# Kernel optimization log

Hardware: AMD Instinct MI355X
Metric: run time of the kernel (lower is better)

The kernel has to match this reference:

```python
import jax, jax.numpy as jnp
import numpy as np

EPS = 1e-12  # F.normalize eps
WIN_SIZE = 200
WIN_STEP = 30  # eval mode (training uses 10)
N_WIN = 30     # 31 windows from length-1100 axis, last one dropped


def setup_inputs() -> dict:
    key = jax.random.key(0)
    ks = jax.random.split(key, 6)
    dim, K, out_dim = 128, 64, 256
    N, H, W = 8, 16, 900
    s = 1.0 / np.sqrt(dim)
    return {
        "x": jax.random.normal(ks[0], (N, dim, H, W), dtype=jnp.float32),
        "cluster_centers": jax.random.uniform(ks[1], (K, dim), dtype=jnp.float32),
        "conv_w": jax.random.normal(ks[2], (K, dim), dtype=jnp.float32) * s,
        "conv_b": jax.random.normal(ks[3], (K,), dtype=jnp.float32) * s,
        "mlp_w": jax.random.normal(ks[4], (out_dim, K * dim), dtype=jnp.float32) * s,
        "mlp_b": jax.random.normal(ks[5], (out_dim,), dtype=jnp.float32) * s,
    }


def _l2norm(v, axis):
    return v / jnp.clip(jnp.linalg.norm(v, axis=axis, keepdims=True), EPS)


def reference(x, cluster_centers, conv_w, conv_b, mlp_w, mlp_b):
    N, C, H, W = x.shape
    K = conv_w.shape[0]
    # 1x1 conv -> soft assignment, softmax over clusters (dim=1 after view(N,K,HW))
    logits = jnp.einsum('nchw,kc->nkhw', x, conv_w) + conv_b[None, :, None, None]
    a = jax.nn.softmax(logits, axis=1)  # (N,K,H,W)
    # Fused weighted residual sum over H (torch sums dim=-2 of (N,K,C,H,W)):
    # vlad_pre[n,k,c,w] = sum_h a[n,k,h,w]*x[n,c,h,w] - centers[k,c]*sum_h a[n,k,h,w]
    wx = jnp.einsum('nkhw,nchw->nkcw', a, x)               # (N,K,C,W)
    asum = a.sum(axis=2)                                    # (N,K,W)
    res = wx - cluster_centers[None, :, :, None] * asum[:, :, None, :]
    # circular pad along yaw: [800:] ++ all ++ [:100] -> length 1100
    res = jnp.concatenate([res[..., 800:], res, res[..., :100]], axis=-1)
    # sliding-window sum, size 200 step 30, drop last window -> 30 windows
    cs = jnp.cumsum(res, axis=-1)
    cs = jnp.concatenate([jnp.zeros(res.shape[:-1] + (1,), res.dtype), cs], axis=-1)
    starts = jnp.arange(N_WIN) * WIN_STEP
    win = cs[..., starts + WIN_SIZE] - cs[..., starts]      # (N,K,C,30)
    vlad = jnp.transpose(win, (0, 3, 1, 2)).reshape(N * N_WIN, K, C)
    vlad = _l2norm(vlad, axis=2)                            # intra-norm per cluster
    vlad = _l2norm(vlad.reshape(N * N_WIN, K * C), axis=1)  # global norm
    out = vlad @ mlp_w.T + mlp_b
    out = _l2norm(out, axis=1)
    return out.reshape(N, N_WIN, -1)
```

## Files before the change

kernel.cpp:

```cpp
#include <hip/hip_runtime.h>
#include <cstddef>

#define EPSF 1e-12f
#define NCB 90
#define NT 30
#define ODIM 256
#define DDIM 8192

typedef unsigned short u16;
typedef __attribute__((ext_vector_type(8))) short short8;
typedef __attribute__((ext_vector_type(4))) float float4v;

__device__ inline u16 f2bf(float f) {
  union { float f; unsigned u; } v; v.f = f;
  unsigned r = v.u + 0x7FFFu + ((v.u >> 16) & 1u);
  return (u16)(r >> 16);
}
__device__ inline float bf2f(u16 h) {
  union { unsigned u; float f; } v; v.u = ((unsigned)h) << 16;
  return v.f;
}

__global__ __launch_bounds__(256, 3) void k1_assign(
    const float* __restrict__ x,
    const float* __restrict__ conv_w,
    const float* __restrict__ conv_b,
    float* __restrict__ P,
    float* __restrict__ PA)
{
  __shared__ u16 xtf[4160];
  __shared__ u16 xf[5120];
  __shared__ float As[64 * 33];
  __shared__ u16 afr[2048];
  __shared__ float invs[32];
  __shared__ float pasum[256];

  const int bx0 = blockIdx.x;
  const int id = (bx0 & 7) * 90 + (bx0 >> 3);
  const int n = id / NCB, cb = id - n * NCB;
  const int t = threadIdx.x;
  const int lane = t & 63;
  const int w = t >> 6;

  const float* xn = x + (size_t)n * 1843200 + cb * 10;

  const int colt = w & 1;
  const int kt0 = w >> 1;
  const float bk0 = conv_b[kt0 * 16 + (lane & 15)];
  const float bk1 = conv_b[(kt0 + 2) * 16 + (lane & 15)];

  short8 w0h[4], w0l[4], w1h[4], w1l[4];
  {
    int kr0 = kt0 * 16 + (lane & 15);
    int kr1 = kr0 + 32;
    int cbase = (lane >> 4) << 3;
#pragma unroll
    for (int cb32 = 0; cb32 < 4; ++cb32) {
      const float* wp0 = conv_w + (size_t)kr0 * 128 + cb32 * 32 + cbase;
      const float* wp1 = conv_w + (size_t)kr1 * 128 + cb32 * 32 + cbase;
      union { u16 u[8]; short8 v; } hh, ll;
#pragma unroll
      for (int j = 0; j < 8; ++j) {
        float fv = wp0[j];
        u16 h = f2bf(fv);
        hh.u[j] = h;
        ll.u[j] = f2bf(fv - bf2f(h));
      }
      w0h[cb32] = hh.v; w0l[cb32] = ll.v;
#pragma unroll
      for (int j = 0; j < 8; ++j) {
        float fv = wp1[j];
        u16 h = f2bf(fv);
        hh.u[j] = h;
        ll.u[j] = f2bf(fv - bf2f(h));
      }
      w1h[cb32] = hh.v; w1l[cb32] = ll.v;
    }
  }

  float4v pacc[8];
#pragma unroll
  for (int i = 0; i < 8; ++i) pacc[i] = (float4v){0.f, 0.f, 0.f, 0.f};
  float pak = 0.f;

  float2 xr[8];
#pragma unroll
  for (int s = 0; s < 8; ++s) {
    int e2 = t + 256 * s;
    int c = e2 >> 4, p = e2 & 15;
    int cl = 2 * p;
    int h = cl / 10, wi = cl - 10 * h;
    xr[s] = *(const float2*)(xn + (size_t)c * 14400 + h * 900 + wi);
  }

  for (int cc = 0; cc < 5; ++cc) {
    __syncthreads();
#pragma unroll
    for (int s = 0; s < 8; ++s) {
      int e2 = t + 256 * s;
      int c = e2 >> 4, p = e2 & 15;
      int cl = 2 * p;
      u16 h0 = f2bf(xr[s].x), h1 = f2bf(xr[s].y);
      int ip = (c >> 4) * 640 + (p >> 2) * 160 + (c & 15) * 8 + (cl & 7);
      ushort2 pr; pr.x = h0; pr.y = h1;
      *(ushort2*)&xf[ip] = pr;
      int F = (p >> 3) * 4 + (c >> 5);
      int L = (((c >> 3) & 3) << 4) + (cl & 15);
      int i0 = F * 520 + L * 8 + (c & 7);
      xtf[i0] = h0;
      xtf[i0 + 8] = h1;
    }
    if (cc < 4) {
#pragma unroll
      for (int s = 0; s < 8; ++s) {
        int e2 = t + 256 * s;
        int c = e2 >> 4, p = e2 & 15;
        int g = (cc + 1) * 32 + 2 * p;
        int h = g / 10, wi = g - 10 * h;
        xr[s] = *(const float2*)(xn + (size_t)c * 14400 + h * 900 + wi);
      }
    }
    __syncthreads();

    {
      float4v d0 = (float4v){0.f, 0.f, 0.f, 0.f};
      float4v d1 = (float4v){0.f, 0.f, 0.f, 0.f};
#pragma unroll
      for (int cb32 = 0; cb32 < 4; ++cb32) {
        short8 xa = *(short8*)&xtf[(colt * 4 + cb32) * 520 + lane * 8];
        d0 = __builtin_amdgcn_mfma_f32_16x16x32_bf16(xa, w0h[cb32], d0, 0, 0, 0);
        d0 = __builtin_amdgcn_mfma_f32_16x16x32_bf16(xa, w0l[cb32], d0, 0, 0, 0);
        d1 = __builtin_amdgcn_mfma_f32_16x16x32_bf16(xa, w1h[cb32], d1, 0, 0, 0);
        d1 = __builtin_amdgcn_mfma_f32_16x16x32_bf16(xa, w1l[cb32], d1, 0, 0, 0);
      }
      int colb = colt * 16 + ((lane >> 4) << 2);
      int kr0 = kt0 * 16 + (lane & 15);
      int kr1 = kr0 + 32;
#pragma unroll
      for (int r = 0; r < 4; ++r) {
        As[kr0 * 33 + colb + r] = d0[r] + bk0;
        As[kr1 * 33 + colb + r] = d1[r] + bk1;
      }
    }
    __syncthreads();

    {
      const int col8 = lane & 7;
      const int kq = lane >> 3;
      const int colg = w * 8 + col8;
      float m = -3.4e38f;
#pragma unroll
      for (int i = 0; i < 8; ++i) m = fmaxf(m, As[(kq * 8 + i) * 33 + colg]);
      m = fmaxf(m, __shfl_xor(m, 8));
      m = fmaxf(m, __shfl_xor(m, 16));
      m = fmaxf(m, __shfl_xor(m, 32));
      float s = 0.f;
#pragma unroll
      for (int i = 0; i < 8; ++i) {
        int a = (kq * 8 + i) * 33 + colg;
        float e = __expf(As[a] - m);
        As[a] = e;
        s += e;
      }
      s += __shfl_xor(s, 8);
      s += __shfl_xor(s, 16);
      s += __shfl_xor(s, 32);
      if (kq == 0) invs[w * 8 + col8] = 1.f / s;
    }
    {
      union { u16 u[8]; short8 v; } cvt;
      float paks = 0.f;
#pragma unroll
      for (int j = 0; j < 8; ++j) {
        float a = As[lane * 33 + w * 8 + j] * invs[w * 8 + j];
        paks += a;
        cvt.u[j] = f2bf(a);
      }
      pak += paks;
      int dst = ((lane >> 4) * 64 + (w << 4) + (lane & 15)) * 8;
      *(short8*)&afr[dst] = cvt.v;
    }
    __syncthreads();

    {
      short8 aa = *(short8*)&afr[(w * 64 + lane) * 8];
#pragma unroll
      for (int ct = 0; ct < 8; ++ct) {
        short8 xb = *(short8*)&xf[ct * 640 + (lane >> 4) * 160 + (lane & 15) * 8];
        pacc[ct] = __builtin_amdgcn_mfma_f32_16x16x32_bf16(aa, xb, pacc[ct], 0, 0, 0);
      }
    }
  }

  float* Pp = P + (size_t)(n * NCB + cb) * DDIM;
  {
    int krow = w * 16 + ((lane >> 4) << 2);
    int c0 = lane & 15;
#pragma unroll
    for (int ct = 0; ct < 8; ++ct)
#pragma unroll
      for (int r = 0; r < 4; ++r)
        Pp[(krow + r) * 128 + ct * 16 + c0] = pacc[ct][r];
  }
  pasum[t] = pak;
  __syncthreads();
  if (t < 64)
    PA[(size_t)(n * NCB + cb) * 64 + t] =
        pasum[t] + pasum[64 + t] + pasum[128 + t] + pasum[192 + t];
}

__global__ __launch_bounds__(256) void k2_vlad(
    const float* __restrict__ P, const float* __restrict__ PA,
    const float* __restrict__ centers, u16* __restrict__ vlad16,
    float* __restrict__ gss)
{
  __shared__ float Ak[8];
  __shared__ float red[4];
  const int bx0 = blockIdx.x;
  const int id = (bx0 & 7) * 240 + (bx0 >> 3);
  const int n = id / 240;
  const int rem = id - n * 240;
  const int wt = rem >> 3, eb = rem & 7;
  const int win = n * NT + wt;
  const int t = threadIdx.x;

  if (t < 32) {
    int kk = t >> 2, ii = t & 3;
    float s = 0.f;
#pragma unroll
    for (int ss = 0; ss < 5; ++ss) {
      int i = ii + 4 * ss;
      int cb = (3 * wt + 80 + i) % 90;
      s += PA[((size_t)n * NCB + cb) * 64 + eb * 8 + kk];
    }
    s += __shfl_xor(s, 1);
    s += __shfl_xor(s, 2);
    if (ii == 0) Ak[kk] = s;
  }
  __syncthreads();

  const int e0 = eb * 1024 + t * 4;
  const float* base = P + (size_t)n * NCB * DDIM + e0;
  float v[4];
#pragma unroll
  for (int j = 0; j < 4; ++j) v[j] = 0.f;
#pragma unroll 5
  for (int i = 0; i < 20; ++i) {
    int cb = (3 * wt + 80 + i) % 90;
    float4 u0 = *(const float4*)(base + (size_t)cb * DDIM);
    v[0] += u0.x; v[1] += u0.y; v[2] += u0.z; v[3] += u0.w;
  }

  const float A = Ak[t >> 5];
  const float* ce = centers + e0;
  float ss8 = 0.f;
#pragma unroll
  for (int j = 0; j < 4; ++j) {
    float val = v[j] - ce[j] * A;
    v[j] = val;
    ss8 += val * val;
  }
  float ssg = ss8;
  ssg += __shfl_xor(ssg, 1);
  ssg += __shfl_xor(ssg, 2);
  ssg += __shfl_xor(ssg, 4);
  ssg += __shfl_xor(ssg, 8);
  ssg += __shfl_xor(ssg, 16);
  float rn = 1.f / fmaxf(sqrtf(ssg), EPSF);
  float ts = ss8 * rn * rn;
  ts += __shfl_xor(ts, 1);
  ts += __shfl_xor(ts, 2);
  ts += __shfl_xor(ts, 4);
  ts += __shfl_xor(ts, 8);
  ts += __shfl_xor(ts, 16);
  ts += __shfl_xor(ts, 32);
  if ((t & 63) == 0) red[t >> 6] = ts;
  __syncthreads();
  if (t == 0) gss[(size_t)win * 8 + eb] = red[0] + red[1] + red[2] + red[3];

  union { u16 u[4]; ushort4 v4; } o;
#pragma unroll
  for (int j = 0; j < 4; ++j) o.u[j] = f2bf(v[j] * rn);
  *(ushort4*)(vlad16 + (size_t)win * DDIM + e0) = o.v4;
}

__global__ __launch_bounds__(256) void k3_gemm(
    const u16* __restrict__ vlad16, const float* __restrict__ gss,
    const float* __restrict__ mlp_w, float* __restrict__ part)
{
  __shared__ float ga[48];
  const int bx = blockIdx.x;
  const int xcd = bx & 7;
  const int q = bx >> 3;
  const int rtg = q % 5;
  const int h = (q / 5) * 8 + xcd;
  const int ot = h & 1;
  const int ks = h >> 1;
  const int t = threadIdx.x;
  const int lane = t & 63;
  const int w = t >> 6;

  if (t < 48) {
    int r = rtg * 48 + t;
    float s = 0.f;
#pragma unroll
    for (int j = 0; j < 8; ++j) s += gss[(size_t)r * 8 + j];
    ga[t] = 1.f / fmaxf(sqrtf(s), EPSF);
  }
  __syncthreads();

  const int m = lane & 15;
  const int kg = lane >> 4;
  const int d0 = ks * 256 + kg * 8;
  const u16* a0 = vlad16 + (size_t)(rtg * 48 + m) * DDIM + d0;

  float4v acc[3][2];
#pragma unroll
  for (int mi = 0; mi < 3; ++mi)
#pragma unroll
    for (int i = 0; i < 2; ++i) acc[mi][i] = (float4v){0.f, 0.f, 0.f, 0.f};

#pragma unroll
  for (int ko = 0; ko < 8; ++ko) {
    short8 a[3];
#pragma unroll
    for (int mi = 0; mi < 3; ++mi)
      a[mi] = *(const short8*)(a0 + (size_t)(mi * 16) * DDIM + ko * 32);
#pragma unroll
    for (int nt = 0; nt < 2; ++nt) {
      int o = ot * 128 + w * 32 + nt * 16 + m;
      const float* wrow = mlp_w + (size_t)o * DDIM + d0 + ko * 32;
      float4 u0 = *(const float4*)wrow;
      float4 u1 = *(const float4*)(wrow + 4);
      union { u16 u[8]; short8 v; } bb;
      bb.u[0] = f2bf(u0.x); bb.u[1] = f2bf(u0.y); bb.u[2] = f2bf(u0.z); bb.u[3] = f2bf(u0.w);
      bb.u[4] = f2bf(u1.x); bb.u[5] = f2bf(u1.y); bb.u[6] = f2bf(u1.z); bb.u[7] = f2bf(u1.w);
#pragma unroll
      for (int mi = 0; mi < 3; ++mi)
        acc[mi][nt] = __builtin_amdgcn_mfma_f32_16x16x32_bf16(a[mi], bb.v, acc[mi][nt], 0, 0, 0);
    }
  }

  float* pp = part + ((size_t)ks * 240 + rtg * 48) * ODIM;
#pragma unroll
  for (int mi = 0; mi < 3; ++mi)
#pragma unroll
    for (int nt = 0; nt < 2; ++nt) {
      int o = ot * 128 + w * 32 + nt * 16 + m;
#pragma unroll
      for (int r = 0; r < 4; ++r) {
        int rl = mi * 16 + kg * 4 + r;
        pp[rl * ODIM + o] = acc[mi][nt][r] * ga[rl];
      }
    }
}

__global__ __launch_bounds__(1024) void k4_out(
    const float* __restrict__ part, const float* __restrict__ bias,
    float* __restrict__ out)
{
  __shared__ float acc[4][256];
  __shared__ float red[4];
  const int r = blockIdx.x;
  const int t = threadIdx.x;
  const int o = t & 255, sq = t >> 8;

  float v = 0.f;
#pragma unroll
  for (int s = 0; s < 8; ++s)
    v += part[((size_t)(sq * 8 + s) * 240 + r) * ODIM + o];
  acc[sq][o] = v;
  __syncthreads();

  float ss = 0.f;
  if (t < 256) {
    v = acc[0][o] + acc[1][o] + acc[2][o] + acc[3][o] + bias[o];
    ss = v * v;
    ss += __shfl_xor(ss, 32);
    ss += __shfl_xor(ss, 16);
    ss += __shfl_xor(ss, 8);
    ss += __shfl_xor(ss, 4);
    ss += __shfl_xor(ss, 2);
    ss += __shfl_xor(ss, 1);
    if ((t & 63) == 0) red[t >> 6] = ss;
  }
  __syncthreads();
  if (t < 256) {
    float total = red[0] + red[1] + red[2] + red[3];
    out[(size_t)r * ODIM + o] = v / fmaxf(sqrtf(total), EPSF);
  }
}

extern "C" void kernel_launch(void* const* d_in, const int* in_sizes, int n_in,
                              void* d_out, int out_size, void* d_ws, size_t ws_size,
                              hipStream_t stream) {
  const float* x       = (const float*)d_in[0];
  const float* centers = (const float*)d_in[1];
  const float* conv_w  = (const float*)d_in[2];
  const float* conv_b  = (const float*)d_in[3];
  const float* mlp_w   = (const float*)d_in[4];
  const float* mlp_b   = (const float*)d_in[5];
  float* out = (float*)d_out;

  float* ws     = (float*)d_ws;
  float* P      = ws;
  float* PA     = ws + 5898240;
  u16*   vlad16 = (u16*)(ws + 5944320);
  float* gss    = (float*)(ws + 6927360);
  float* part   = ws;

  k1_assign<<<dim3(8 * NCB),    dim3(256),  0, stream>>>(x, conv_w, conv_b, P, PA);
  k2_vlad  <<<dim3(8 * NT * 8), dim3(256),  0, stream>>>(P, PA, centers, vlad16, gss);
  k3_gemm  <<<dim3(320),        dim3(256),  0, stream>>>(vlad16, gss, mlp_w, part);
  k4_out   <<<dim3(240),        dim3(1024), 0, stream>>>(part, mlp_b, out);
}
```

Measured before the change: 172.2 us.

## Split k1_assign work across 8 waves with 512-thread blocks

Doubles k1_assign's block size from 256 to 512 threads and splits per-wave work in half. Each wave now computes one 16-cluster tile of logits, handles 4 columns in the softmax, and runs 4 of the 8 channel tiles in the weighted-sum MFMA. Weight loading uses float4 vector loads, and the block-index mapping to (n, cb) is simplified. The aim is more waves per block to hide latency and lighter register pressure per thread, at the cost of larger blocks, possibly fewer resident blocks per CU, and an extra shuffle stage in the softmax.

```diff
diff --git a/kernel.cpp b/kernel.cpp
--- a/kernel.cpp
+++ b/kernel.cpp
@@ -21,7 +21,7 @@
   return v.f;
 }
 
-__global__ __launch_bounds__(256, 3) void k1_assign(
+__global__ __launch_bounds__(512, 2) void k1_assign(
     const float* __restrict__ x,
     const float* __restrict__ conv_w,
     const float* __restrict__ conv_b,
@@ -33,60 +33,51 @@
   __shared__ float As[64 * 33];
   __shared__ u16 afr[2048];
   __shared__ float invs[32];
-  __shared__ float pasum[256];
+  __shared__ float pasum[512];
 
   const int bx0 = blockIdx.x;
-  const int id = (bx0 & 7) * 90 + (bx0 >> 3);
-  const int n = id / NCB, cb = id - n * NCB;
+  const int n = bx0 & 7;
+  const int cb = bx0 >> 3;
   const int t = threadIdx.x;
   const int lane = t & 63;
-  const int w = t >> 6;
+  const int w8 = t >> 6;
 
   const float* xn = x + (size_t)n * 1843200 + cb * 10;
 
-  const int colt = w & 1;
-  const int kt0 = w >> 1;
-  const float bk0 = conv_b[kt0 * 16 + (lane & 15)];
-  const float bk1 = conv_b[(kt0 + 2) * 16 + (lane & 15)];
-
-  short8 w0h[4], w0l[4], w1h[4], w1l[4];
+  const int colt = w8 & 1;
+  const int kt = w8 >> 1;
+  const int kr = kt * 16 + (lane & 15);
+  const float bk = conv_b[kr];
+
+  short8 wh[4], wl[4];
   {
-    int kr0 = kt0 * 16 + (lane & 15);
-    int kr1 = kr0 + 32;
-    int cbase = (lane >> 4) << 3;
+    const int cbase = (lane >> 4) << 3;
 #pragma unroll
     for (int cb32 = 0; cb32 < 4; ++cb32) {
-      const float* wp0 = conv_w + (size_t)kr0 * 128 + cb32 * 32 + cbase;
-      const float* wp1 = conv_w + (size_t)kr1 * 128 + cb32 * 32 + cbase;
+      const float* wp = conv_w + (size_t)kr * 128 + cb32 * 32 + cbase;
+      float4 u0 = *(const float4*)wp;
+      float4 u1 = *(const float4*)(wp + 4);
+      float fv[8] = {u0.x, u0.y, u0.z, u0.w, u1.x, u1.y, u1.z, u1.w};
       union { u16 u[8]; short8 v; } hh, ll;
 #pragma unroll
       for (int j = 0; j < 8; ++j) {
-        float fv = wp0[j];
-        u16 h = f2bf(fv);
+        u16 h = f2bf(fv[j]);
         hh.u[j] = h;
-        ll.u[j] = f2bf(fv - bf2f(h));
-      }
-      w0h[cb32] = hh.v; w0l[cb32] = ll.v;
-#pragma unroll
-      for (int j = 0; j < 8; ++j) {
-        float fv = wp1[j];
-        u16 h = f2bf(fv);
-        hh.u[j] = h;
-        ll.u[j] = f2bf(fv - bf2f(h));
-      }
-      w1h[cb32] = hh.v; w1l[cb32] = ll.v;
-    }
-  }
-
-  float4v pacc[8];
-#pragma unroll
-  for (int i = 0; i < 8; ++i) pacc[i] = (float4v){0.f, 0.f, 0.f, 0.f};
+        ll.u[j] = f2bf(fv[j] - bf2f(h));
+      }
+      wh[cb32] = hh.v; wl[cb32] = ll.v;
+    }
+  }
+
+  float4v pacc[4];
+#pragma unroll
+  for (int i = 0; i < 4; ++i) pacc[i] = (float4v){0.f, 0.f, 0.f, 0.f};
   float pak = 0.f;
 
-  float2 xr[8];
-#pragma unroll
-  for (int s = 0; s < 8; ++s) {
-    int e2 = t + 256 * s;
+  float2 xr[4];
+#pragma unroll
+  for (int s = 0; s < 4; ++s) {
+    int e2 = t + 512 * s;
     int c = e2 >> 4, p = e2 & 15;
     int cl = 2 * p;
     int h = cl / 10, wi = cl - 10 * h;
@@ -96,8 +87,8 @@
   for (int cc = 0; cc < 5; ++cc) {
     __syncthreads();
 #pragma unroll
-    for (int s = 0; s < 8; ++s) {
-      int e2 = t + 256 * s;
+    for (int s = 0; s < 4; ++s) {
+      int e2 = t + 512 * s;
       int c = e2 >> 4, p = e2 & 15;
       int cl = 2 * p;
       u16 h0 = f2bf(xr[s].x), h1 = f2bf(xr[s].y);
@@ -112,8 +103,8 @@
     }
     if (cc < 4) {
 #pragma unroll
-      for (int s = 0; s < 8; ++s) {
-        int e2 = t + 256 * s;
+      for (int s = 0; s < 4; ++s) {
+        int e2 = t + 512 * s;
         int c = e2 >> 4, p = e2 & 15;
         int g = (cc + 1) * 32 + 2 * p;
         int h = g / 10, wi = g - 10 * h;
@@ -124,89 +115,88 @@
 
     {
       float4v d0 = (float4v){0.f, 0.f, 0.f, 0.f};
-      float4v d1 = (float4v){0.f, 0.f, 0.f, 0.f};
 #pragma unroll
       for (int cb32 = 0; cb32 < 4; ++cb32) {
         short8 xa = *(short8*)&xtf[(colt * 4 + cb32) * 520 + lane * 8];
-        d0 = __builtin_amdgcn_mfma_f32_16x16x32_bf16(xa, w0h[cb32], d0, 0, 0, 0);
-        d0 = __builtin_amdgcn_mfma_f32_16x16x32_bf16(xa, w0l[cb32], d0, 0, 0, 0);
-        d1 = __builtin_amdgcn_mfma_f32_16x16x32_bf16(xa, w1h[cb32], d1, 0, 0, 0);
-        d1 = __builtin_amdgcn_mfma_f32_16x16x32_bf16(xa, w1l[cb32], d1, 0, 0, 0);
+        d0 = __builtin_amdgcn_mfma_f32_16x16x32_bf16(xa, wh[cb32], d0, 0, 0, 0);
+        d0 = __builtin_amdgcn_mfma_f32_16x16x32_bf16(xa, wl[cb32], d0, 0, 0, 0);
       }
       int colb = colt * 16 + ((lane >> 4) << 2);
-      int kr0 = kt0 * 16 + (lane & 15);
-      int kr1 = kr0 + 32;
-#pragma unroll
-      for (int r = 0; r < 4; ++r) {
-        As[kr0 * 33 + colb + r] = d0[r] + bk0;
-        As[kr1 * 33 + colb + r] = d1[r] + bk1;
-      }
+#pragma unroll
+      for (int r = 0; r < 4; ++r)
+        As[kr * 33 + colb + r] = d0[r] + bk;
     }
     __syncthreads();
 
     {
-      const int col8 = lane & 7;
-      const int kq = lane >> 3;
-      const int colg = w * 8 + col8;
+      const int col4 = lane & 3;
+      const int kq = lane >> 2;
+      const int colg = w8 * 4 + col4;
       float m = -3.4e38f;
 #pragma unroll
-      for (int i = 0; i < 8; ++i) m = fmaxf(m, As[(kq * 8 + i) * 33 + colg]);
+      for (int i = 0; i < 4; ++i) m = fmaxf(m, As[(kq * 4 + i) * 33 + colg]);
+      m = fmaxf(m, __shfl_xor(m, 4));
       m = fmaxf(m, __shfl_xor(m, 8));
       m = fmaxf(m, __shfl_xor(m, 16));
       m = fmaxf(m, __shfl_xor(m, 32));
       float s = 0.f;
 #pragma unroll
-      for (int i = 0; i < 8; ++i) {
-        int a = (kq * 8 + i) * 33 + colg;
+      for (int i = 0; i < 4; ++i) {
+        int a = (kq * 4 + i) * 33 + colg;
         float e = __expf(As[a] - m);
         As[a] = e;
         s += e;
       }
+      s += __shfl_xor(s, 4);
       s += __shfl_xor(s, 8);
       s += __shfl_xor(s, 16);
       s += __shfl_xor(s, 32);
-      if (kq == 0) invs[w * 8 + col8] = 1.f / s;
+      if (kq == 0) invs[colg] = 1.f / s;
     }
     {
-      union { u16 u[8]; short8 v; } cvt;
+      union { u16 u[4]; ushort4 v; } cvt;
       float paks = 0.f;
 #pragma unroll
-      for (int j = 0; j < 8; ++j) {
-        float a = As[lane * 33 + w * 8 + j] * invs[w * 8 + j];
+      for (int j = 0; j < 4; ++j) {
+        float a = As[lane * 33 + w8 * 4 + j] * invs[w8 * 4 + j];
         paks += a;
         cvt.u[j] = f2bf(a);
       }
       pak += paks;
-      int dst = ((lane >> 4) * 64 + (w << 4) + (lane & 15)) * 8;
-      *(short8*)&afr[dst] = cvt.v;
+      int dst = ((lane >> 4) * 64 + ((w8 >> 1) << 4) + (lane & 15)) * 8 + (w8 & 1) * 4;
+      *(ushort4*)&afr[dst] = cvt.v;
     }
     __syncthreads();
 
     {
-      short8 aa = *(short8*)&afr[(w * 64 + lane) * 8];
-#pragma unroll
-      for (int ct = 0; ct < 8; ++ct) {
+      short8 aa = *(short8*)&afr[((w8 >> 1) * 64 + lane) * 8];
+#pragma unroll
+      for (int c4 = 0; c4 < 4; ++c4) {
+        int ct = (w8 & 1) * 4 + c4;
         short8 xb = *(short8*)&xf[ct * 640 + (lane >> 4) * 160 + (lane & 15) * 8];
-        pacc[ct] = __builtin_amdgcn_mfma_f32_16x16x32_bf16(aa, xb, pacc[ct], 0, 0, 0);
+        pacc[c4] = __builtin_amdgcn_mfma_f32_16x16x32_bf16(aa, xb, pacc[c4], 0, 0, 0);
       }
     }
   }
 
   float* Pp = P + (size_t)(n * NCB + cb) * DDIM;
   {
-    int krow = w * 16 + ((lane >> 4) << 2);
-    int c0 = lane & 15;
-#pragma unroll
-    for (int ct = 0; ct < 8; ++ct)
+    int krow = (w8 >> 1) * 16 + ((lane >> 4) << 2);
+    int c0 = (w8 & 1) * 64 + (lane & 15);
+#pragma unroll
+    for (int c4 = 0; c4 < 4; ++c4)
 #pragma unroll
       for (int r = 0; r < 4; ++r)
-        Pp[(krow + r) * 128 + ct * 16 + c0] = pacc[ct][r];
+        Pp[(krow + r) * 128 + c0 + c4 * 16] = pacc[c4][r];
   }
   pasum[t] = pak;
   __syncthreads();
-  if (t < 64)
-    PA[(size_t)(n * NCB + cb) * 64 + t] =
-        pasum[t] + pasum[64 + t] + pasum[128 + t] + pasum[192 + t];
+  if (t < 64) {
+    float s = 0.f;
+#pragma unroll
+    for (int i = 0; i < 8; ++i) s += pasum[t + 64 * i];
+    PA[(size_t)(n * NCB + cb) * 64 + t] = s;
+  }
 }
 
 __global__ __launch_bounds__(256) void k2_vlad(
@@ -409,7 +399,7 @@
   float* gss    = (float*)(ws + 6927360);
   float* part   = ws;
 
-  k1_assign<<<dim3(8 * NCB),    dim3(256),  0, stream>>>(x, conv_w, conv_b, P, PA);
+  k1_assign<<<dim3(8 * NCB),    dim3(512),  0, stream>>>(x, conv_w, conv_b, P, PA);
   k2_vlad  <<<dim3(8 * NT * 8), dim3(256),  0, stream>>>(P, PA, centers, vlad16, gss);
   k3_gemm  <<<dim3(320),        dim3(256),  0, stream>>>(vlad16, gss, mlp_w, part);
   k4_out   <<<dim3(240),        dim3(1024), 0, stream>>>(part, mlp_b, out);
```

Result: faster. 161.7 us (-6.1%).
